# Kernel tuning notes

Hardware: AMD Instinct MI355X
Metric: run time of the kernel (lower is better)

The kernel has to match this reference:

```python
import jax, jax.numpy as jnp
import numpy as np

B, F, H, L, K = 16384, 1024, 1024, 256, 7

def _lin(key, fi, fo, lead=()):
    k1, k2 = jax.random.split(key)
    s = 1.0 / np.sqrt(fi)
    W = jax.random.uniform(k1, lead + (fi, fo), jnp.float32, -s, s)
    b = jax.random.uniform(k2, lead + (fo,), jnp.float32, -s, s)
    return W, b

def setup_inputs() -> dict:
    ks = jax.random.split(jax.random.key(0), 16)
    x = jax.random.normal(ks[0], (B, F), jnp.float32)
    t = jax.random.randint(ks[1], (B,), 0, K, jnp.int32)
    y = jax.random.normal(ks[2], (B,), jnp.float32)
    d = jax.random.normal(ks[3], (B,), jnp.float32)
    tw0, tb0 = _lin(ks[4], F, L)
    tw1, tb1 = _lin(ks[5], L, L)
    tw2, tb2 = _lin(ks[6], L, K)
    yw0, yb0 = _lin(ks[7], F, H)
    yw1, yb1 = _lin(ks[8], H, H)
    yhW, yhb = _lin(ks[9], H, 2, (K,))
    dw0, db0 = _lin(ks[10], F, H)
    dw1, db1 = _lin(ks[11], H, H)
    dhW, dhb = _lin(ks[12], H, 2, (K,))
    zw0, zb0 = _lin(ks[13], F + 2, H)
    zw1, zb1 = _lin(ks[14], H, H)
    zhW, zhb = _lin(ks[15], H, 2 * L, (K,))
    return dict(x=x, t=t, y=y, d=d, tw0=tw0, tb0=tb0, tw1=tw1, tb1=tb1, tw2=tw2, tb2=tb2,
                yw0=yw0, yb0=yb0, yw1=yw1, yb1=yb1, yhW=yhW, yhb=yhb,
                dw0=dw0, db0=db0, dw1=dw1, db1=db1, dhW=dhW, dhb=dhb,
                zw0=zw0, zb0=zb0, zw1=zw1, zb1=zb1, zhW=zhW, zhb=zhb)

def _mlp2(x, w0, b0, w1, b1):
    # FullyConnected([in, H, H], final_activation=ELU)
    return jax.nn.elu(jax.nn.elu(x @ w0 + b0) @ w1 + b1)

def _select(hidden, t, hW, hb):
    # dense compute of all K treatment heads, then per-row gather by t
    all_out = jnp.einsum('bh,khd->bkd', hidden, hW) + hb  # [B, K, D]
    return jnp.take_along_axis(all_out, t[:, None, None], axis=1)[:, 0]

def _normal_head(sel):
    # pyro NormalNet head on a scalar outcome
    loc = jnp.clip(sel[:, 0:1], -1e6, 1e6)
    scale = jnp.minimum(jax.nn.softplus(sel[:, 1:2]) + 1e-3, 1e6)
    return loc, scale

def _diagnormal_head(sel):
    loc = jnp.clip(sel[:, :L], -100.0, 100.0)
    scale = jnp.minimum(jax.nn.softplus(sel[:, L:]) + 0.001, 100.0)
    return loc, scale

def reference(x, t, y, d, tw0, tb0, tw1, tb1, tw2, tb2,
              yw0, yb0, yw1, yb1, yhW, yhb,
              dw0, db0, dw1, db1, dhW, dhb,
              zw0, zb0, zw1, zb1, zhW, zhb):
    # t_nn: MultinormNet, ELU final activation then clamp(-10, 10)
    t_logits = jnp.clip(jax.nn.elu(_mlp2(x, tw0, tb0, tw1, tb1) @ tw2 + tb2), -10.0, 10.0)
    # y_dist(t, x)
    hy = _mlp2(x, yw0, yb0, yw1, yb1)
    y_loc, y_scale = _normal_head(_select(hy, t, yhW, yhb))
    # d_dist(t, x)
    hd = _mlp2(x, dw0, db0, dw1, db1)
    d_loc, d_scale = _normal_head(_select(hd, t, dhW, dhb))
    # z_dist(y, d, t, x): hidden from cat([y, d, x])
    hz = _mlp2(jnp.concatenate([y[:, None], d[:, None], x], axis=-1), zw0, zb0, zw1, zb1)
    z_loc, z_scale = _diagnormal_head(_select(hz, t, zhW, zhb))
    # [B, K + 4 + 2L]
    return jnp.concatenate([t_logits, y_loc, y_scale, d_loc, d_scale, z_loc, z_scale], axis=-1)
```

## Files before the change

kernel.cpp:

```cpp
#include <hip/hip_runtime.h>
#include <hip/hip_bf16.h>
#include <cstdint>
#include <cstddef>

typedef __hip_bfloat16 bf16;
typedef __bf16 bf16x8 __attribute__((ext_vector_type(8)));
typedef float f32x4 __attribute__((ext_vector_type(4)));

#define DEVFN static __device__ __forceinline__

DEVFN void async16(const void* g, void* l) {
  __builtin_amdgcn_global_load_lds(
      (const __attribute__((address_space(1))) uint32_t*)g,
      (__attribute__((address_space(3))) uint32_t*)l, 16, 0, 0);
}

DEVFN float eluf(float v) { return v > 0.f ? v : expm1f(v); }
DEVFN float softplusf(float x) {
  return x > 0.f ? x + log1pf(expf(-x)) : log1pf(expf(x));
}

template <int KITERS>
DEVFN void kloop128(const bf16* gA0, const bf16* gA1, const bf16* gB0,
                    const bf16* gB1, bf16* lA0, bf16* lA1, bf16* lB0, bf16* lB1,
                    const bf16* aBase, const bf16* bBase, f32x4 (&acc)[4][4]) {
  for (int kt = 0; kt < KITERS; ++kt) {
    async16(gA0, lA0); async16(gA1, lA1);
    async16(gB0, lB0); async16(gB1, lB1);
    gA0 += 32; gA1 += 32; gB0 += 32; gB1 += 32;
    __syncthreads();
    bf16x8 af[4], bfv[4];
#pragma unroll
    for (int r = 0; r < 4; ++r) af[r] = *(const bf16x8*)(aBase + r * 512);
#pragma unroll
    for (int c = 0; c < 4; ++c) bfv[c] = *(const bf16x8*)(bBase + c * 512);
#pragma unroll
    for (int r = 0; r < 4; ++r)
#pragma unroll
      for (int c = 0; c < 4; ++c)
        acc[r][c] = __builtin_amdgcn_mfma_f32_16x16x32_bf16(af[r], bfv[c], acc[r][c], 0, 0, 0);
    __syncthreads();
  }
}

__global__ __launch_bounds__(256) void cvt_x_k(const float* __restrict__ src,
                                               bf16* __restrict__ dst) {
  size_t i = ((size_t)blockIdx.x * 256 + threadIdx.x) * 8;
  float4 v0 = *(const float4*)(src + i);
  float4 v1 = *(const float4*)(src + i + 4);
  union { bf16 h[8]; uint4 u; } o;
  o.h[0] = __float2bfloat16(v0.x); o.h[1] = __float2bfloat16(v0.y);
  o.h[2] = __float2bfloat16(v0.z); o.h[3] = __float2bfloat16(v0.w);
  o.h[4] = __float2bfloat16(v1.x); o.h[5] = __float2bfloat16(v1.y);
  o.h[6] = __float2bfloat16(v1.z); o.h[7] = __float2bfloat16(v1.w);
  *(uint4*)(dst + i) = o.u;
}

DEVFN void transpose_tile(const float* src, bf16* dst, int R, int C) {
  __shared__ float tile[32][33];
  const int c0 = blockIdx.x * 32, r0 = blockIdx.y * 32;
  const int tx = threadIdx.x & 31, ty = threadIdx.x >> 5;
#pragma unroll
  for (int rr = ty; rr < 32; rr += 8)
    tile[rr][tx] = src[(size_t)(r0 + rr) * C + c0 + tx];
  __syncthreads();
#pragma unroll
  for (int rr = ty; rr < 32; rr += 8)
    dst[(size_t)(c0 + rr) * R + r0 + tx] = __float2bfloat16(tile[tx][rr]);
}

__global__ __launch_bounds__(256) void trcvt_k(const float* __restrict__ src,
                                               bf16* __restrict__ dst, int R, int C) {
  transpose_tile(src + (size_t)blockIdx.z * R * C,
                 dst + (size_t)blockIdx.z * R * C, R, C);
}

__global__ __launch_bounds__(256) void trcvt4_k(
    const float* __restrict__ s0, const float* __restrict__ s1,
    const float* __restrict__ s2, const float* __restrict__ s3,
    bf16* __restrict__ dst) {
  const int z = blockIdx.z;
  const float* src = (z == 0) ? s0 : (z == 1) ? s1 : (z == 2) ? s2 : s3;
  const int C = (z == 3) ? 256 : 1024;
  if ((int)blockIdx.x * 32 >= C) return;
  transpose_tile(src, dst + (size_t)z * 1024 * 1024, 1024, C);
}

__global__ __launch_bounds__(256) void trcvt3_k(
    const float* __restrict__ s0, const float* __restrict__ s1,
    const float* __restrict__ s2, bf16* __restrict__ dst) {
  const int z = blockIdx.z;
  const float* src = (z == 0) ? s0 : (z == 1) ? s1 : s2;
  transpose_tile(src, dst + (size_t)z * 1024 * 1024, 1024, 1024);
}

__global__ __launch_bounds__(256) void biascat_k(
    const float* __restrict__ yb0, const float* __restrict__ db0,
    const float* __restrict__ zb0, const float* __restrict__ tb0,
    const float* __restrict__ zw0, const float* __restrict__ yb1,
    const float* __restrict__ db1, const float* __restrict__ zb1,
    float* __restrict__ biasAll, float* __restrict__ r0All,
    float* __restrict__ r1All, float* __restrict__ biasL2) {
  int i = blockIdx.x * 256 + threadIdx.x;
  if (i >= 3328) return;
  float b;
  if (i < 1024) b = yb0[i];
  else if (i < 2048) b = db0[i - 1024];
  else if (i < 3072) b = zb0[i - 2048];
  else b = tb0[i - 3072];
  biasAll[i] = b;
  bool inz = (i >= 2048 && i < 3072);
  r0All[i] = inz ? zw0[i - 2048] : 0.f;
  r1All[i] = inz ? zw0[1024 + (i - 2048)] : 0.f;
  if (i < 3072)
    biasL2[i] = (i < 1024) ? yb1[i] : (i < 2048) ? db1[i - 1024] : zb1[i - 2048];
}

__global__ __launch_bounds__(256) void bucketize_k(const int* __restrict__ t,
                                                   int* __restrict__ cnt,
                                                   int* __restrict__ pos) {
  int b = blockIdx.x * 256 + threadIdx.x;
  pos[b] = atomicAdd(&cnt[t[b]], 1);
}
__global__ void segk(const int* __restrict__ cnt, int* __restrict__ seg) {
  if (threadIdx.x == 0) {
    int s = 0;
    for (int k = 0; k < 7; ++k) { seg[k] = s; s += cnt[k]; }
    seg[7] = s;
  }
}
__global__ __launch_bounds__(256) void rankk(const int* __restrict__ t,
                                             const int* __restrict__ pos,
                                             const int* __restrict__ seg,
                                             int* __restrict__ rank,
                                             int* __restrict__ sids) {
  int b = blockIdx.x * 256 + threadIdx.x;
  int r = seg[t[b]] + pos[b];
  rank[b] = r;
  sids[r] = b;
}

__global__ __launch_bounds__(256) void gemm_l1_k(
    const bf16* __restrict__ A, const bf16* __restrict__ Bt,
    const float* __restrict__ biasAll, const float* __restrict__ r0All,
    const float* __restrict__ r1All, const float* __restrict__ yv,
    const float* __restrict__ dv, bf16* __restrict__ a1y,
    bf16* __restrict__ a1d, bf16* __restrict__ a1z, bf16* __restrict__ ht1) {
  __shared__ bf16 As[128 * 32];
  __shared__ bf16 Bs[128 * 32];
  const int tid = threadIdx.x, lane = tid & 63, wid = tid >> 6;
  const int wm = wid >> 1, wn = wid & 1, quad = lane >> 4, l15 = lane & 15;
  const int bm0 = blockIdx.y * 128, bn0 = blockIdx.x * 128;
  const int sr = tid >> 2, sc = (tid & 3) * 8;
  f32x4 acc[4][4] = {};
  kloop128<32>(A + (size_t)(bm0 + sr) * 1024 + sc,
               A + (size_t)(bm0 + 64 + sr) * 1024 + sc,
               Bt + (size_t)(bn0 + sr) * 1024 + sc,
               Bt + (size_t)(bn0 + 64 + sr) * 1024 + sc,
               &As[tid * 8], &As[2048 + tid * 8], &Bs[tid * 8], &Bs[2048 + tid * 8],
               &As[(wm * 64 + l15) * 32 + quad * 8],
               &Bs[(wn * 64 + l15) * 32 + quad * 8], acc);
  const int g = bn0 >> 10;
  bf16* dst = (g == 0) ? a1y : (g == 1) ? a1d : (g == 2) ? a1z : ht1;
  const int ldc = (g == 3) ? 256 : 1024;
  const int colb = bn0 - g * 1024;
  float bv[4], z0[4], z1[4];
#pragma unroll
  for (int c = 0; c < 4; ++c) {
    int gn = bn0 + wn * 64 + c * 16 + l15;
    bv[c] = biasAll[gn]; z0[c] = r0All[gn]; z1[c] = r1All[gn];
  }
#pragma unroll
  for (int r = 0; r < 4; ++r) {
#pragma unroll
    for (int q = 0; q < 4; ++q) {
      int gm = bm0 + wm * 64 + r * 16 + quad * 4 + q;
      float yy = yv[gm], dd = dv[gm];
#pragma unroll
      for (int c = 0; c < 4; ++c) {
        float v = acc[r][c][q] + bv[c] + yy * z0[c] + dd * z1[c];
        dst[(size_t)gm * ldc + colb + wn * 64 + c * 16 + l15] = __float2bfloat16(eluf(v));
      }
    }
  }
}

__global__ __launch_bounds__(256) void gemm_l2_k(
    const bf16* __restrict__ a1y, const bf16* __restrict__ a1d,
    const bf16* __restrict__ a1z, const bf16* __restrict__ Bt,
    const float* __restrict__ biasL2, bf16* __restrict__ hyd,
    bf16* __restrict__ hzg, const int* __restrict__ rank) {
  __shared__ bf16 As[128 * 32];
  __shared__ bf16 Bs[128 * 32];
  const int tid = threadIdx.x, lane = tid & 63, wid = tid >> 6;
  const int wm = wid >> 1, wn = wid & 1, quad = lane >> 4, l15 = lane & 15;
  const int bm0 = blockIdx.y * 128, bn0 = blockIdx.x * 128;
  const int g = bn0 >> 10;
  const bf16* A = (g == 0) ? a1y : (g == 1) ? a1d : a1z;
  const int sr = tid >> 2, sc = (tid & 3) * 8;
  f32x4 acc[4][4] = {};
  kloop128<32>(A + (size_t)(bm0 + sr) * 1024 + sc,
               A + (size_t)(bm0 + 64 + sr) * 1024 + sc,
               Bt + (size_t)(bn0 + sr) * 1024 + sc,
               Bt + (size_t)(bn0 + 64 + sr) * 1024 + sc,
               &As[tid * 8], &As[2048 + tid * 8], &Bs[tid * 8], &Bs[2048 + tid * 8],
               &As[(wm * 64 + l15) * 32 + quad * 8],
               &Bs[(wn * 64 + l15) * 32 + quad * 8], acc);
  float bv[4];
#pragma unroll
  for (int c = 0; c < 4; ++c) bv[c] = biasL2[bn0 + wn * 64 + c * 16 + l15];
#pragma unroll
  for (int r = 0; r < 4; ++r) {
#pragma unroll
    for (int q = 0; q < 4; ++q) {
      int gm = bm0 + wm * 64 + r * 16 + quad * 4 + q;
      size_t rowoff = (g == 2) ? (size_t)rank[gm] * 1024 + (size_t)(bn0 - 2048)
                               : (size_t)gm * 2048 + (size_t)bn0;
      bf16* dst = (g == 2) ? hzg : hyd;
#pragma unroll
      for (int c = 0; c < 4; ++c) {
        float v = acc[r][c][q] + bv[c];
        dst[rowoff + wn * 64 + c * 16 + l15] = __float2bfloat16(eluf(v));
      }
    }
  }
}

__global__ __launch_bounds__(256) void gemm_t1_k(const bf16* __restrict__ A,
                                                 const bf16* __restrict__ Bt,
                                                 const float* __restrict__ bias,
                                                 bf16* __restrict__ C) {
  __shared__ bf16 As[128 * 32];
  __shared__ bf16 Bs[128 * 32];
  const int tid = threadIdx.x, lane = tid & 63, wid = tid >> 6;
  const int wm = wid >> 1, wn = wid & 1, quad = lane >> 4, l15 = lane & 15;
  const int bm0 = blockIdx.y * 128, bn0 = blockIdx.x * 128;
  const int sr = tid >> 2, sc = (tid & 3) * 8;
  f32x4 acc[4][4] = {};
  kloop128<8>(A + (size_t)(bm0 + sr) * 256 + sc,
              A + (size_t)(bm0 + 64 + sr) * 256 + sc,
              Bt + (size_t)(bn0 + sr) * 256 + sc,
              Bt + (size_t)(bn0 + 64 + sr) * 256 + sc,
              &As[tid * 8], &As[2048 + tid * 8], &Bs[tid * 8], &Bs[2048 + tid * 8],
              &As[(wm * 64 + l15) * 32 + quad * 8],
              &Bs[(wn * 64 + l15) * 32 + quad * 8], acc);
  float bv[4];
#pragma unroll
  for (int c = 0; c < 4; ++c) bv[c] = bias[bn0 + wn * 64 + c * 16 + l15];
#pragma unroll
  for (int r = 0; r < 4; ++r)
#pragma unroll
    for (int q = 0; q < 4; ++q) {
      int gm = bm0 + wm * 64 + r * 16 + quad * 4 + q;
#pragma unroll
      for (int c = 0; c < 4; ++c)
        C[(size_t)gm * 256 + bn0 + wn * 64 + c * 16 + l15] =
            __float2bfloat16(eluf(acc[r][c][q] + bv[c]));
    }
}

__global__ __launch_bounds__(256) void zhead_k(
    const bf16* __restrict__ hzg, const bf16* __restrict__ zhWt,
    const float* __restrict__ zhb, const int* __restrict__ seg,
    const int* __restrict__ cnts, const int* __restrict__ sids,
    float* __restrict__ out) {
  const int kb = blockIdx.z;
  const int cnt = cnts[kb];
  const int bm0 = blockIdx.y * 128;
  if (bm0 >= cnt) return;
  __shared__ bf16 As[128 * 32];
  __shared__ bf16 Bs[64 * 32];
  const int tid = threadIdx.x, lane = tid & 63, wid = tid >> 6;
  const int wm = wid >> 1, wn = wid & 1, quad = lane >> 4, l15 = lane & 15;
  const int n0 = blockIdx.x * 64;
  const int base = seg[kb];
  const int sr = tid >> 2, sc = (tid & 3) * 8;
  int r0i = bm0 + sr;      if (r0i >= cnt) r0i = cnt - 1;
  int r1i = bm0 + 64 + sr; if (r1i >= cnt) r1i = cnt - 1;
  const bf16* gA0 = hzg + (size_t)(base + r0i) * 1024 + sc;
  const bf16* gA1 = hzg + (size_t)(base + r1i) * 1024 + sc;
  const bf16* gB0 = zhWt + (size_t)kb * 512 * 1024 + (size_t)(n0 + sr) * 1024 + sc;
  bf16 *lA0 = &As[tid * 8], *lA1 = &As[2048 + tid * 8], *lB0 = &Bs[tid * 8];
  const bf16* aBase = &As[(wm * 64 + l15) * 32 + quad * 8];
  const bf16* bBase = &Bs[(wn * 32 + l15) * 32 + quad * 8];
  f32x4 acc[4][2] = {};
  for (int kt = 0; kt < 32; ++kt) {
    async16(gA0, lA0); async16(gA1, lA1); async16(gB0, lB0);
    gA0 += 32; gA1 += 32; gB0 += 32;
    __syncthreads();
    bf16x8 af[4], bfv[2];
#pragma unroll
    for (int r = 0; r < 4; ++r) af[r] = *(const bf16x8*)(aBase + r * 512);
#pragma unroll
    for (int c = 0; c < 2; ++c) bfv[c] = *(const bf16x8*)(bBase + c * 512);
#pragma unroll
    for (int r = 0; r < 4; ++r)
#pragma unroll
      for (int c = 0; c < 2; ++c)
        acc[r][c] = __builtin_amdgcn_mfma_f32_16x16x32_bf16(af[r], bfv[c], acc[r][c], 0, 0, 0);
    __syncthreads();
  }
  const float* bias = zhb + (size_t)kb * 512;
  float bv[2]; int gnn[2];
#pragma unroll
  for (int c = 0; c < 2; ++c) {
    gnn[c] = n0 + wn * 32 + c * 16 + l15;
    bv[c] = bias[gnn[c]];
  }
#pragma unroll
  for (int r = 0; r < 4; ++r)
#pragma unroll
    for (int q = 0; q < 4; ++q) {
      int lm = bm0 + wm * 64 + r * 16 + quad * 4 + q;
      if (lm < cnt) {
        int gm = sids[base + lm];
        size_t ob = (size_t)gm * 523 + 11;
#pragma unroll
        for (int c = 0; c < 2; ++c) {
          float v = acc[r][c][q] + bv[c];
          int n = gnn[c];
          out[ob + n] = (n < 256) ? fminf(fmaxf(v, -100.f), 100.f)
                                  : fminf(softplusf(v) + 0.001f, 100.f);
        }
      }
    }
}

__global__ __launch_bounds__(256) void yd_head_k(
    const bf16* __restrict__ hyd, const int* __restrict__ t,
    const float* __restrict__ yhW, const float* __restrict__ yhb,
    const float* __restrict__ dhW, const float* __restrict__ dhb,
    float* __restrict__ out) {
  const int wv = threadIdx.x >> 6, lane = threadIdx.x & 63;
  const int b = blockIdx.x * 4 + wv;
  const int tb = t[b];
  const float* yW = yhW + (size_t)tb * 2048;
  const float* dW = dhW + (size_t)tb * 2048;
  float s0 = 0.f, s1 = 0.f, s2 = 0.f, s3 = 0.f;
  for (int i = lane; i < 1024; i += 64) {
    float a = __bfloat162float(hyd[(size_t)b * 2048 + i]);
    float c = __bfloat162float(hyd[(size_t)b * 2048 + 1024 + i]);
    s0 += a * yW[2 * i]; s1 += a * yW[2 * i + 1];
    s2 += c * dW[2 * i]; s3 += c * dW[2 * i + 1];
  }
#pragma unroll
  for (int off = 32; off > 0; off >>= 1) {
    s0 += __shfl_down(s0, off); s1 += __shfl_down(s1, off);
    s2 += __shfl_down(s2, off); s3 += __shfl_down(s3, off);
  }
  if (lane == 0) {
    size_t o = (size_t)b * 523;
    out[o + 7] = fminf(fmaxf(s0 + yhb[tb * 2], -1e6f), 1e6f);
    out[o + 8] = fminf(softplusf(s1 + yhb[tb * 2 + 1]) + 1e-3f, 1e6f);
    out[o + 9] = fminf(fmaxf(s2 + dhb[tb * 2], -1e6f), 1e6f);
    out[o + 10] = fminf(softplusf(s3 + dhb[tb * 2 + 1]) + 1e-3f, 1e6f);
  }
}

__global__ __launch_bounds__(256) void tlogits_k(
    const bf16* __restrict__ ht2, const float* __restrict__ tw2,
    const float* __restrict__ tb2, float* __restrict__ out) {
  const int wv = threadIdx.x >> 6, lane = threadIdx.x & 63;
  const int b = blockIdx.x * 4 + wv;
  float h[4];
#pragma unroll
  for (int j = 0; j < 4; ++j)
    h[j] = __bfloat162float(ht2[(size_t)b * 256 + lane * 4 + j]);
  float pp[7];
#pragma unroll
  for (int kk = 0; kk < 7; ++kk) {
    float s = 0.f;
#pragma unroll
    for (int j = 0; j < 4; ++j) s += h[j] * tw2[(lane * 4 + j) * 7 + kk];
    pp[kk] = s;
  }
#pragma unroll
  for (int kk = 0; kk < 7; ++kk)
#pragma unroll
    for (int off = 32; off > 0; off >>= 1) pp[kk] += __shfl_down(pp[kk], off);
  if (lane == 0) {
#pragma unroll
    for (int kk = 0; kk < 7; ++kk) {
      float v = eluf(pp[kk] + tb2[kk]);
      out[(size_t)b * 523 + kk] = fminf(fmaxf(v, -10.f), 10.f);
    }
  }
}

extern "C" void kernel_launch(void* const* d_in, const int* in_sizes, int n_in,
                              void* d_out, int out_size, void* d_ws, size_t ws_size,
                              hipStream_t stream) {
  const float* x   = (const float*)d_in[0];
  const int*   t   = (const int*)d_in[1];
  const float* yv  = (const float*)d_in[2];
  const float* dv  = (const float*)d_in[3];
  const float* tw0 = (const float*)d_in[4];
  const float* tb0 = (const float*)d_in[5];
  const float* tw1 = (const float*)d_in[6];
  const float* tb1 = (const float*)d_in[7];
  const float* tw2 = (const float*)d_in[8];
  const float* tb2 = (const float*)d_in[9];
  const float* yw0 = (const float*)d_in[10];
  const float* yb0 = (const float*)d_in[11];
  const float* yw1 = (const float*)d_in[12];
  const float* yb1 = (const float*)d_in[13];
  const float* yhW = (const float*)d_in[14];
  const float* yhb = (const float*)d_in[15];
  const float* dw0 = (const float*)d_in[16];
  const float* db0 = (const float*)d_in[17];
  const float* dw1 = (const float*)d_in[18];
  const float* db1 = (const float*)d_in[19];
  const float* dhW = (const float*)d_in[20];
  const float* dhb = (const float*)d_in[21];
  const float* zw0 = (const float*)d_in[22];
  const float* zb0 = (const float*)d_in[23];
  const float* zw1 = (const float*)d_in[24];
  const float* zb1 = (const float*)d_in[25];
  const float* zhW = (const float*)d_in[26];
  const float* zhb = (const float*)d_in[27];
  float* out = (float*)d_out;

  const int B = 16384;
  char* p = (char*)d_ws;
  auto take = [&](size_t bytes) {
    char* r = p;
    p += (bytes + 255) & ~(size_t)255;
    return r;
  };
  bf16*  BtL1    = (bf16*)take((size_t)3328 * 1024 * 2);
  bf16*  BtL2    = (bf16*)take((size_t)3072 * 1024 * 2);
  bf16*  tw1t    = (bf16*)take((size_t)256 * 256 * 2);
  bf16*  zhWt    = (bf16*)take((size_t)7 * 512 * 1024 * 2);
  float* biasAll = (float*)take(3328 * 4);
  float* r0All   = (float*)take(3328 * 4);
  float* r1All   = (float*)take(3328 * 4);
  float* biasL2  = (float*)take(3072 * 4);
  int*   cnt     = (int*)take(8 * 4);
  int*   seg     = (int*)take(8 * 4);
  int*   pos     = (int*)take((size_t)B * 4);
  int*   rank    = (int*)take((size_t)B * 4);
  int*   sids    = (int*)take((size_t)B * 4);
  bf16*  xb      = (bf16*)take((size_t)B * 1024 * 2);
  bf16*  a1y     = (bf16*)take((size_t)B * 1024 * 2);
  bf16*  a1d     = (bf16*)take((size_t)B * 1024 * 2);
  bf16*  a1z     = (bf16*)take((size_t)B * 1024 * 2);
  bf16*  ht1     = (bf16*)take((size_t)B * 256 * 2);
  bf16*  hyd     = (bf16*)take((size_t)B * 2048 * 2);
  bf16*  hzg     = xb;
  bf16*  ht2     = a1y;

  hipMemsetAsync(cnt, 0, 8 * 4, stream);
  bucketize_k<<<B / 256, 256, 0, stream>>>(t, cnt, pos);
  segk<<<1, 64, 0, stream>>>(cnt, seg);
  rankk<<<B / 256, 256, 0, stream>>>(t, pos, seg, rank, sids);
  cvt_x_k<<<(B * 1024) / (256 * 8), 256, 0, stream>>>(x, xb);
  trcvt4_k<<<dim3(32, 32, 4), 256, 0, stream>>>(yw0, dw0, zw0 + 2 * 1024, tw0, BtL1);
  trcvt3_k<<<dim3(32, 32, 3), 256, 0, stream>>>(yw1, dw1, zw1, BtL2);
  trcvt_k<<<dim3(8, 8, 1), 256, 0, stream>>>(tw1, tw1t, 256, 256);
  trcvt_k<<<dim3(16, 32, 7), 256, 0, stream>>>(zhW, zhWt, 1024, 512);
  biascat_k<<<13, 256, 0, stream>>>(yb0, db0, zb0, tb0, zw0, yb1, db1, zb1,
                                    biasAll, r0All, r1All, biasL2);
  gemm_l1_k<<<dim3(26, 128), 256, 0, stream>>>(xb, BtL1, biasAll, r0All, r1All,
                                               yv, dv, a1y, a1d, a1z, ht1);
  gemm_l2_k<<<dim3(24, 128), 256, 0, stream>>>(a1y, a1d, a1z, BtL2, biasL2,
                                               hyd, hzg, rank);
  gemm_t1_k<<<dim3(2, 128), 256, 0, stream>>>(ht1, tw1t, tb1, ht2);
  zhead_k<<<dim3(8, 24, 7), 256, 0, stream>>>(hzg, zhWt, zhb, seg, cnt, sids, out);
  yd_head_k<<<B / 4, 256, 0, stream>>>(hyd, t, yhW, yhb, dhW, dhb, out);
  tlogits_k<<<B / 4, 256, 0, stream>>>(ht2, tw2, tb2, out);
}
```

Baseline: 777.2 us.

## Merge prep, layer-2/t1 GEMMs and head kernels; add XCD-aware tile mapping

Folds the x conversion, all weight transposes and the bias packing into one prep kernel. Merges the t-branch layer-1 GEMM into the layer-2 GEMM launch and fuses the y/d head and t-logit kernels into one. Remaps GEMM block IDs so each XCD works on a contiguous band of M tiles, which is meant to improve L2 reuse of A rows. This cuts launch count and tail effects, at the cost of a runtime K-loop count (less unrolling) and a separate ht2 buffer instead of reusing a1y.

```diff
diff --git a/kernel.cpp b/kernel.cpp
--- a/kernel.cpp
+++ b/kernel.cpp
@@ -20,11 +20,11 @@
   return x > 0.f ? x + log1pf(expf(-x)) : log1pf(expf(x));
 }
 
-template <int KITERS>
-DEVFN void kloop128(const bf16* gA0, const bf16* gA1, const bf16* gB0,
-                    const bf16* gB1, bf16* lA0, bf16* lA1, bf16* lB0, bf16* lB1,
-                    const bf16* aBase, const bf16* bBase, f32x4 (&acc)[4][4]) {
-  for (int kt = 0; kt < KITERS; ++kt) {
+DEVFN void kloop(const bf16* gA0, const bf16* gA1, const bf16* gB0,
+                 const bf16* gB1, bf16* lA0, bf16* lA1, bf16* lB0, bf16* lB1,
+                 const bf16* aBase, const bf16* bBase, f32x4 (&acc)[4][4],
+                 int kiters) {
+  for (int kt = 0; kt < kiters; ++kt) {
     async16(gA0, lA0); async16(gA1, lA1);
     async16(gB0, lB0); async16(gB1, lB1);
     gA0 += 32; gA1 += 32; gB0 += 32; gB1 += 32;
@@ -43,22 +43,9 @@
   }
 }
 
-__global__ __launch_bounds__(256) void cvt_x_k(const float* __restrict__ src,
-                                               bf16* __restrict__ dst) {
-  size_t i = ((size_t)blockIdx.x * 256 + threadIdx.x) * 8;
-  float4 v0 = *(const float4*)(src + i);
-  float4 v1 = *(const float4*)(src + i + 4);
-  union { bf16 h[8]; uint4 u; } o;
-  o.h[0] = __float2bfloat16(v0.x); o.h[1] = __float2bfloat16(v0.y);
-  o.h[2] = __float2bfloat16(v0.z); o.h[3] = __float2bfloat16(v0.w);
-  o.h[4] = __float2bfloat16(v1.x); o.h[5] = __float2bfloat16(v1.y);
-  o.h[6] = __float2bfloat16(v1.z); o.h[7] = __float2bfloat16(v1.w);
-  *(uint4*)(dst + i) = o.u;
-}
-
-DEVFN void transpose_tile(const float* src, bf16* dst, int R, int C) {
+DEVFN void transpose_tile(const float* src, bf16* dst, int R, int C, int bx, int by) {
   __shared__ float tile[32][33];
-  const int c0 = blockIdx.x * 32, r0 = blockIdx.y * 32;
+  const int c0 = bx * 32, r0 = by * 32;
   const int tx = threadIdx.x & 31, ty = threadIdx.x >> 5;
 #pragma unroll
   for (int rr = ty; rr < 32; rr += 8)
@@ -69,51 +56,78 @@
     dst[(size_t)(c0 + rr) * R + r0 + tx] = __float2bfloat16(tile[tx][rr]);
 }
 
-__global__ __launch_bounds__(256) void trcvt_k(const float* __restrict__ src,
-                                               bf16* __restrict__ dst, int R, int C) {
-  transpose_tile(src + (size_t)blockIdx.z * R * C,
-                 dst + (size_t)blockIdx.z * R * C, R, C);
-}
-
-__global__ __launch_bounds__(256) void trcvt4_k(
-    const float* __restrict__ s0, const float* __restrict__ s1,
-    const float* __restrict__ s2, const float* __restrict__ s3,
-    bf16* __restrict__ dst) {
-  const int z = blockIdx.z;
-  const float* src = (z == 0) ? s0 : (z == 1) ? s1 : (z == 2) ? s2 : s3;
-  const int C = (z == 3) ? 256 : 1024;
-  if ((int)blockIdx.x * 32 >= C) return;
-  transpose_tile(src, dst + (size_t)z * 1024 * 1024, 1024, C);
-}
-
-__global__ __launch_bounds__(256) void trcvt3_k(
-    const float* __restrict__ s0, const float* __restrict__ s1,
-    const float* __restrict__ s2, bf16* __restrict__ dst) {
-  const int z = blockIdx.z;
-  const float* src = (z == 0) ? s0 : (z == 1) ? s1 : s2;
-  transpose_tile(src, dst + (size_t)z * 1024 * 1024, 1024, 1024);
-}
-
-__global__ __launch_bounds__(256) void biascat_k(
+__global__ __launch_bounds__(256) void prep_all_k(
+    const float* __restrict__ x, bf16* __restrict__ xb,
+    const float* __restrict__ yw0, const float* __restrict__ dw0,
+    const float* __restrict__ zw0, const float* __restrict__ tw0,
+    bf16* __restrict__ BtL1,
+    const float* __restrict__ yw1, const float* __restrict__ dw1,
+    const float* __restrict__ zw1, bf16* __restrict__ BtL2,
+    const float* __restrict__ tw1, bf16* __restrict__ tw1t,
+    const float* __restrict__ zhW, bf16* __restrict__ zhWt,
     const float* __restrict__ yb0, const float* __restrict__ db0,
     const float* __restrict__ zb0, const float* __restrict__ tb0,
-    const float* __restrict__ zw0, const float* __restrict__ yb1,
-    const float* __restrict__ db1, const float* __restrict__ zb1,
+    const float* __restrict__ yb1, const float* __restrict__ db1,
+    const float* __restrict__ zb1,
     float* __restrict__ biasAll, float* __restrict__ r0All,
     float* __restrict__ r1All, float* __restrict__ biasL2) {
-  int i = blockIdx.x * 256 + threadIdx.x;
-  if (i >= 3328) return;
-  float b;
-  if (i < 1024) b = yb0[i];
-  else if (i < 2048) b = db0[i - 1024];
-  else if (i < 3072) b = zb0[i - 2048];
-  else b = tb0[i - 3072];
-  biasAll[i] = b;
-  bool inz = (i >= 2048 && i < 3072);
-  r0All[i] = inz ? zw0[i - 2048] : 0.f;
-  r1All[i] = inz ? zw0[1024 + (i - 2048)] : 0.f;
-  if (i < 3072)
-    biasL2[i] = (i < 1024) ? yb1[i] : (i < 2048) ? db1[i - 1024] : zb1[i - 2048];
+  int l = blockIdx.x;
+  if (l < 8192) {
+    size_t i = ((size_t)l * 256 + threadIdx.x) * 8;
+    float4 v0 = *(const float4*)(x + i);
+    float4 v1 = *(const float4*)(x + i + 4);
+    union { bf16 h[8]; uint4 u; } o;
+    o.h[0] = __float2bfloat16(v0.x); o.h[1] = __float2bfloat16(v0.y);
+    o.h[2] = __float2bfloat16(v0.z); o.h[3] = __float2bfloat16(v0.w);
+    o.h[4] = __float2bfloat16(v1.x); o.h[5] = __float2bfloat16(v1.y);
+    o.h[6] = __float2bfloat16(v1.z); o.h[7] = __float2bfloat16(v1.w);
+    *(uint4*)(xb + i) = o.u;
+    return;
+  }
+  l -= 8192;
+  if (l < 4096) {
+    int z = l >> 10, rem = l & 1023, bx = rem & 31, by = rem >> 5;
+    const float* src = (z == 0) ? yw0 : (z == 1) ? dw0 : (z == 2) ? zw0 + 2048 : tw0;
+    int C = (z == 3) ? 256 : 1024;
+    if (bx * 32 < C)
+      transpose_tile(src, BtL1 + (size_t)z * 1024 * 1024, 1024, C, bx, by);
+    return;
+  }
+  l -= 4096;
+  if (l < 3072) {
+    int z = l >> 10, rem = l & 1023, bx = rem & 31, by = rem >> 5;
+    const float* src = (z == 0) ? yw1 : (z == 1) ? dw1 : zw1;
+    transpose_tile(src, BtL2 + (size_t)z * 1024 * 1024, 1024, 1024, bx, by);
+    return;
+  }
+  l -= 3072;
+  if (l < 64) {
+    transpose_tile(tw1, tw1t, 256, 256, l & 7, l >> 3);
+    return;
+  }
+  l -= 64;
+  if (l < 3584) {
+    int z = l >> 9, rem = l & 511, bx = rem & 15, by = rem >> 4;
+    transpose_tile(zhW + (size_t)z * 1024 * 512, zhWt + (size_t)z * 512 * 1024,
+                   1024, 512, bx, by);
+    return;
+  }
+  l -= 3584;
+  {
+    int i = l * 256 + threadIdx.x;
+    if (i >= 3328) return;
+    float b;
+    if (i < 1024) b = yb0[i];
+    else if (i < 2048) b = db0[i - 1024];
+    else if (i < 3072) b = zb0[i - 2048];
+    else b = tb0[i - 3072];
+    biasAll[i] = b;
+    bool inz = (i >= 2048 && i < 3072);
+    r0All[i] = inz ? zw0[i - 2048] : 0.f;
+    r1All[i] = inz ? zw0[1024 + (i - 2048)] : 0.f;
+    if (i < 3072)
+      biasL2[i] = (i < 1024) ? yb1[i] : (i < 2048) ? db1[i - 1024] : zb1[i - 2048];
+  }
 }
 
 __global__ __launch_bounds__(256) void bucketize_k(const int* __restrict__ t,
@@ -150,17 +164,21 @@
   __shared__ bf16 Bs[128 * 32];
   const int tid = threadIdx.x, lane = tid & 63, wid = tid >> 6;
   const int wm = wid >> 1, wn = wid & 1, quad = lane >> 4, l15 = lane & 15;
-  const int bm0 = blockIdx.y * 128, bn0 = blockIdx.x * 128;
+  const int id = blockIdx.x;
+  const int xcd = id & 7, lid = id >> 3;
+  const int pass = lid / 208, rem = lid - pass * 208;
+  const int mt = xcd * 16 + pass * 8 + (rem & 7), nt = rem >> 3;
+  const int bm0 = mt * 128, bn0 = nt * 128;
   const int sr = tid >> 2, sc = (tid & 3) * 8;
   f32x4 acc[4][4] = {};
-  kloop128<32>(A + (size_t)(bm0 + sr) * 1024 + sc,
-               A + (size_t)(bm0 + 64 + sr) * 1024 + sc,
-               Bt + (size_t)(bn0 + sr) * 1024 + sc,
-               Bt + (size_t)(bn0 + 64 + sr) * 1024 + sc,
-               &As[tid * 8], &As[2048 + tid * 8], &Bs[tid * 8], &Bs[2048 + tid * 8],
-               &As[(wm * 64 + l15) * 32 + quad * 8],
-               &Bs[(wn * 64 + l15) * 32 + quad * 8], acc);
-  const int g = bn0 >> 10;
+  kloop(A + (size_t)(bm0 + sr) * 1024 + sc,
+        A + (size_t)(bm0 + 64 + sr) * 1024 + sc,
+        Bt + (size_t)(bn0 + sr) * 1024 + sc,
+        Bt + (size_t)(bn0 + 64 + sr) * 1024 + sc,
+        &As[tid * 8], &As[2048 + tid * 8], &Bs[tid * 8], &Bs[2048 + tid * 8],
+        &As[(wm * 64 + l15) * 32 + quad * 8],
+        &Bs[(wn * 64 + l15) * 32 + quad * 8], acc, 32);
+  const int g = nt >> 3;
   bf16* dst = (g == 0) ? a1y : (g == 1) ? a1d : (g == 2) ? a1z : ht1;
   const int ldc = (g == 3) ? 256 : 1024;
   const int colb = bn0 - g * 1024;
@@ -185,38 +203,55 @@
   }
 }
 
-__global__ __launch_bounds__(256) void gemm_l2_k(
+__global__ __launch_bounds__(256) void gemm_l2t_k(
     const bf16* __restrict__ a1y, const bf16* __restrict__ a1d,
-    const bf16* __restrict__ a1z, const bf16* __restrict__ Bt,
-    const float* __restrict__ biasL2, bf16* __restrict__ hyd,
-    bf16* __restrict__ hzg, const int* __restrict__ rank) {
+    const bf16* __restrict__ a1z, const bf16* __restrict__ ht1,
+    const bf16* __restrict__ BtL2, const bf16* __restrict__ tw1t,
+    const float* __restrict__ biasL2, const float* __restrict__ tb1,
+    bf16* __restrict__ hyd, bf16* __restrict__ hzg, bf16* __restrict__ ht2,
+    const int* __restrict__ rank) {
   __shared__ bf16 As[128 * 32];
   __shared__ bf16 Bs[128 * 32];
   const int tid = threadIdx.x, lane = tid & 63, wid = tid >> 6;
   const int wm = wid >> 1, wn = wid & 1, quad = lane >> 4, l15 = lane & 15;
-  const int bm0 = blockIdx.y * 128, bn0 = blockIdx.x * 128;
-  const int g = bn0 >> 10;
-  const bf16* A = (g == 0) ? a1y : (g == 1) ? a1d : a1z;
+  const int id = blockIdx.x;
+  int bm0, bn0, Ka, g;
+  const bf16 *Aptr, *Bptr;
+  if (id < 3072) {
+    const int xcd = id & 7, lid = id >> 3;
+    const int pass = lid / 192, rem = lid - pass * 192;
+    const int mt = xcd * 16 + pass * 8 + (rem & 7), nt = rem >> 3;
+    bm0 = mt * 128; bn0 = nt * 128; Ka = 1024;
+    g = nt >> 3;
+    Aptr = (g == 0) ? a1y : (g == 1) ? a1d : a1z;
+    Bptr = BtL2;
+  } else {
+    const int local = id - 3072;
+    bm0 = (local >> 1) * 128; bn0 = (local & 1) * 128; Ka = 256;
+    g = 3; Aptr = ht1; Bptr = tw1t;
+  }
   const int sr = tid >> 2, sc = (tid & 3) * 8;
   f32x4 acc[4][4] = {};
-  kloop128<32>(A + (size_t)(bm0 + sr) * 1024 + sc,
-               A + (size_t)(bm0 + 64 + sr) * 1024 + sc,
-               Bt + (size_t)(bn0 + sr) * 1024 + sc,
-               Bt + (size_t)(bn0 + 64 + sr) * 1024 + sc,
-               &As[tid * 8], &As[2048 + tid * 8], &Bs[tid * 8], &Bs[2048 + tid * 8],
-               &As[(wm * 64 + l15) * 32 + quad * 8],
-               &Bs[(wn * 64 + l15) * 32 + quad * 8], acc);
+  kloop(Aptr + (size_t)(bm0 + sr) * Ka + sc,
+        Aptr + (size_t)(bm0 + 64 + sr) * Ka + sc,
+        Bptr + (size_t)(bn0 + sr) * Ka + sc,
+        Bptr + (size_t)(bn0 + 64 + sr) * Ka + sc,
+        &As[tid * 8], &As[2048 + tid * 8], &Bs[tid * 8], &Bs[2048 + tid * 8],
+        &As[(wm * 64 + l15) * 32 + quad * 8],
+        &Bs[(wn * 64 + l15) * 32 + quad * 8], acc, Ka >> 5);
+  const float* bias = (g == 3) ? tb1 : biasL2;
   float bv[4];
 #pragma unroll
-  for (int c = 0; c < 4; ++c) bv[c] = biasL2[bn0 + wn * 64 + c * 16 + l15];
+  for (int c = 0; c < 4; ++c) bv[c] = bias[bn0 + wn * 64 + c * 16 + l15];
 #pragma unroll
   for (int r = 0; r < 4; ++r) {
 #pragma unroll
     for (int q = 0; q < 4; ++q) {
       int gm = bm0 + wm * 64 + r * 16 + quad * 4 + q;
-      size_t rowoff = (g == 2) ? (size_t)rank[gm] * 1024 + (size_t)(bn0 - 2048)
-                               : (size_t)gm * 2048 + (size_t)bn0;
-      bf16* dst = (g == 2) ? hzg : hyd;
+      bf16* dst; size_t rowoff;
+      if (g == 2) { dst = hzg; rowoff = (size_t)rank[gm] * 1024 + (size_t)(bn0 - 2048); }
+      else if (g == 3) { dst = ht2; rowoff = (size_t)gm * 256 + bn0; }
+      else { dst = hyd; rowoff = (size_t)gm * 2048 + bn0; }
 #pragma unroll
       for (int c = 0; c < 4; ++c) {
         float v = acc[r][c][q] + bv[c];
@@ -224,39 +259,6 @@
       }
     }
   }
-}
-
-__global__ __launch_bounds__(256) void gemm_t1_k(const bf16* __restrict__ A,
-                                                 const bf16* __restrict__ Bt,
-                                                 const float* __restrict__ bias,
-                                                 bf16* __restrict__ C) {
-  __shared__ bf16 As[128 * 32];
-  __shared__ bf16 Bs[128 * 32];
-  const int tid = threadIdx.x, lane = tid & 63, wid = tid >> 6;
-  const int wm = wid >> 1, wn = wid & 1, quad = lane >> 4, l15 = lane & 15;
-  const int bm0 = blockIdx.y * 128, bn0 = blockIdx.x * 128;
-  const int sr = tid >> 2, sc = (tid & 3) * 8;
-  f32x4 acc[4][4] = {};
-  kloop128<8>(A + (size_t)(bm0 + sr) * 256 + sc,
-              A + (size_t)(bm0 + 64 + sr) * 256 + sc,
-              Bt + (size_t)(bn0 + sr) * 256 + sc,
-              Bt + (size_t)(bn0 + 64 + sr) * 256 + sc,
-              &As[tid * 8], &As[2048 + tid * 8], &Bs[tid * 8], &Bs[2048 + tid * 8],
-              &As[(wm * 64 + l15) * 32 + quad * 8],
-              &Bs[(wn * 64 + l15) * 32 + quad * 8], acc);
-  float bv[4];
-#pragma unroll
-  for (int c = 0; c < 4; ++c) bv[c] = bias[bn0 + wn * 64 + c * 16 + l15];
-#pragma unroll
-  for (int r = 0; r < 4; ++r)
-#pragma unroll
-    for (int q = 0; q < 4; ++q) {
-      int gm = bm0 + wm * 64 + r * 16 + quad * 4 + q;
-#pragma unroll
-      for (int c = 0; c < 4; ++c)
-        C[(size_t)gm * 256 + bn0 + wn * 64 + c * 16 + l15] =
-            __float2bfloat16(eluf(acc[r][c][q] + bv[c]));
-    }
 }
 
 __global__ __launch_bounds__(256) void zhead_k(
@@ -326,63 +328,61 @@
     }
 }
 
-__global__ __launch_bounds__(256) void yd_head_k(
-    const bf16* __restrict__ hyd, const int* __restrict__ t,
-    const float* __restrict__ yhW, const float* __restrict__ yhb,
-    const float* __restrict__ dhW, const float* __restrict__ dhb,
-    float* __restrict__ out) {
-  const int wv = threadIdx.x >> 6, lane = threadIdx.x & 63;
-  const int b = blockIdx.x * 4 + wv;
-  const int tb = t[b];
-  const float* yW = yhW + (size_t)tb * 2048;
-  const float* dW = dhW + (size_t)tb * 2048;
-  float s0 = 0.f, s1 = 0.f, s2 = 0.f, s3 = 0.f;
-  for (int i = lane; i < 1024; i += 64) {
-    float a = __bfloat162float(hyd[(size_t)b * 2048 + i]);
-    float c = __bfloat162float(hyd[(size_t)b * 2048 + 1024 + i]);
-    s0 += a * yW[2 * i]; s1 += a * yW[2 * i + 1];
-    s2 += c * dW[2 * i]; s3 += c * dW[2 * i + 1];
-  }
-#pragma unroll
-  for (int off = 32; off > 0; off >>= 1) {
-    s0 += __shfl_down(s0, off); s1 += __shfl_down(s1, off);
-    s2 += __shfl_down(s2, off); s3 += __shfl_down(s3, off);
-  }
-  if (lane == 0) {
-    size_t o = (size_t)b * 523;
-    out[o + 7] = fminf(fmaxf(s0 + yhb[tb * 2], -1e6f), 1e6f);
-    out[o + 8] = fminf(softplusf(s1 + yhb[tb * 2 + 1]) + 1e-3f, 1e6f);
-    out[o + 9] = fminf(fmaxf(s2 + dhb[tb * 2], -1e6f), 1e6f);
-    out[o + 10] = fminf(softplusf(s3 + dhb[tb * 2 + 1]) + 1e-3f, 1e6f);
-  }
-}
-
-__global__ __launch_bounds__(256) void tlogits_k(
-    const bf16* __restrict__ ht2, const float* __restrict__ tw2,
+__global__ __launch_bounds__(256) void heads_k(
+    const bf16* __restrict__ hyd, const bf16* __restrict__ ht2,
+    const int* __restrict__ t, const float* __restrict__ yhW,
+    const float* __restrict__ yhb, const float* __restrict__ dhW,
+    const float* __restrict__ dhb, const float* __restrict__ tw2,
     const float* __restrict__ tb2, float* __restrict__ out) {
   const int wv = threadIdx.x >> 6, lane = threadIdx.x & 63;
-  const int b = blockIdx.x * 4 + wv;
-  float h[4];
-#pragma unroll
-  for (int j = 0; j < 4; ++j)
-    h[j] = __bfloat162float(ht2[(size_t)b * 256 + lane * 4 + j]);
-  float pp[7];
-#pragma unroll
-  for (int kk = 0; kk < 7; ++kk) {
-    float s = 0.f;
-#pragma unroll
-    for (int j = 0; j < 4; ++j) s += h[j] * tw2[(lane * 4 + j) * 7 + kk];
-    pp[kk] = s;
-  }
-#pragma unroll
-  for (int kk = 0; kk < 7; ++kk)
-#pragma unroll
-    for (int off = 32; off > 0; off >>= 1) pp[kk] += __shfl_down(pp[kk], off);
-  if (lane == 0) {
+  if (blockIdx.x < 4096) {
+    const int b = blockIdx.x * 4 + wv;
+    const int tb = t[b];
+    const float* yW = yhW + (size_t)tb * 2048;
+    const float* dW = dhW + (size_t)tb * 2048;
+    float s0 = 0.f, s1 = 0.f, s2 = 0.f, s3 = 0.f;
+    for (int i = lane; i < 1024; i += 64) {
+      float a = __bfloat162float(hyd[(size_t)b * 2048 + i]);
+      float c = __bfloat162float(hyd[(size_t)b * 2048 + 1024 + i]);
+      s0 += a * yW[2 * i]; s1 += a * yW[2 * i + 1];
+      s2 += c * dW[2 * i]; s3 += c * dW[2 * i + 1];
+    }
+#pragma unroll
+    for (int off = 32; off > 0; off >>= 1) {
+      s0 += __shfl_down(s0, off); s1 += __shfl_down(s1, off);
+      s2 += __shfl_down(s2, off); s3 += __shfl_down(s3, off);
+    }
+    if (lane == 0) {
+      size_t o = (size_t)b * 523;
+      out[o + 7] = fminf(fmaxf(s0 + yhb[tb * 2], -1e6f), 1e6f);
+      out[o + 8] = fminf(softplusf(s1 + yhb[tb * 2 + 1]) + 1e-3f, 1e6f);
+      out[o + 9] = fminf(fmaxf(s2 + dhb[tb * 2], -1e6f), 1e6f);
+      out[o + 10] = fminf(softplusf(s3 + dhb[tb * 2 + 1]) + 1e-3f, 1e6f);
+    }
+  } else {
+    const int b = (blockIdx.x - 4096) * 4 + wv;
+    float h[4];
+#pragma unroll
+    for (int j = 0; j < 4; ++j)
+      h[j] = __bfloat162float(ht2[(size_t)b * 256 + lane * 4 + j]);
+    float pp[7];
 #pragma unroll
     for (int kk = 0; kk < 7; ++kk) {
-      float v = eluf(pp[kk] + tb2[kk]);
-      out[(size_t)b * 523 + kk] = fminf(fmaxf(v, -10.f), 10.f);
+      float s = 0.f;
+#pragma unroll
+      for (int j = 0; j < 4; ++j) s += h[j] * tw2[(lane * 4 + j) * 7 + kk];
+      pp[kk] = s;
+    }
+#pragma unroll
+    for (int kk = 0; kk < 7; ++kk)
+#pragma unroll
+      for (int off = 32; off > 0; off >>= 1) pp[kk] += __shfl_down(pp[kk], off);
+    if (lane == 0) {
+#pragma unroll
+      for (int kk = 0; kk < 7; ++kk) {
+        float v = eluf(pp[kk] + tb2[kk]);
+        out[(size_t)b * 523 + kk] = fminf(fmaxf(v, -10.f), 10.f);
+      }
     }
   }
 }
@@ -446,26 +446,21 @@
   bf16*  a1z     = (bf16*)take((size_t)B * 1024 * 2);
   bf16*  ht1     = (bf16*)take((size_t)B * 256 * 2);
   bf16*  hyd     = (bf16*)take((size_t)B * 2048 * 2);
+  bf16*  ht2     = (bf16*)take((size_t)B * 256 * 2);
   bf16*  hzg     = xb;
-  bf16*  ht2     = a1y;
 
   hipMemsetAsync(cnt, 0, 8 * 4, stream);
   bucketize_k<<<B / 256, 256, 0, stream>>>(t, cnt, pos);
   segk<<<1, 64, 0, stream>>>(cnt, seg);
   rankk<<<B / 256, 256, 0, stream>>>(t, pos, seg, rank, sids);
-  cvt_x_k<<<(B * 1024) / (256 * 8), 256, 0, stream>>>(x, xb);
-  trcvt4_k<<<dim3(32, 32, 4), 256, 0, stream>>>(yw0, dw0, zw0 + 2 * 1024, tw0, BtL1);
-  trcvt3_k<<<dim3(32, 32, 3), 256, 0, stream>>>(yw1, dw1, zw1, BtL2);
-  trcvt_k<<<dim3(8, 8, 1), 256, 0, stream>>>(tw1, tw1t, 256, 256);
-  trcvt_k<<<dim3(16, 32, 7), 256, 0, stream>>>(zhW, zhWt, 1024, 512);
-  biascat_k<<<13, 256, 0, stream>>>(yb0, db0, zb0, tb0, zw0, yb1, db1, zb1,
-                                    biasAll, r0All, r1All, biasL2);
-  gemm_l1_k<<<dim3(26, 128), 256, 0, stream>>>(xb, BtL1, biasAll, r0All, r1All,
-                                               yv, dv, a1y, a1d, a1z, ht1);
-  gemm_l2_k<<<dim3(24, 128), 256, 0, stream>>>(a1y, a1d, a1z, BtL2, biasL2,
-                                               hyd, hzg, rank);
-  gemm_t1_k<<<dim3(2, 128), 256, 0, stream>>>(ht1, tw1t, tb1, ht2);
+  prep_all_k<<<19021, 256, 0, stream>>>(x, xb, yw0, dw0, zw0, tw0, BtL1,
+                                        yw1, dw1, zw1, BtL2, tw1, tw1t, zhW, zhWt,
+                                        yb0, db0, zb0, tb0, yb1, db1, zb1,
+                                        biasAll, r0All, r1All, biasL2);
+  gemm_l1_k<<<3328, 256, 0, stream>>>(xb, BtL1, biasAll, r0All, r1All,
+                                      yv, dv, a1y, a1d, a1z, ht1);
+  gemm_l2t_k<<<3328, 256, 0, stream>>>(a1y, a1d, a1z, ht1, BtL2, tw1t,
+                                       biasL2, tb1, hyd, hzg, ht2, rank);
   zhead_k<<<dim3(8, 24, 7), 256, 0, stream>>>(hzg, zhWt, zhb, seg, cnt, sids, out);
-  yd_head_k<<<B / 4, 256, 0, stream>>>(hyd, t, yhW, yhb, dhW, dhb, out);
-  tlogits_k<<<B / 4, 256, 0, stream>>>(ht2, tw2, tb2, out);
-}
+  heads_k<<<8192, 256, 0, stream>>>(hyd, ht2, t, yhW, yhb, dhW, dhb, tw2, tb2, out);
+}
```

Result: faster. 733.6 us (-5.6%).
